# Kernel tuning notes

Hardware: AMD Instinct MI355X
Metric: run time of the kernel (lower is better)

## Reference

```python
import jax, jax.numpy as jnp
import numpy as np

EMB = 512
HEADS = 8
QKV = 512
WIN = 256  # 'range' init arg, >1 so W = range


def setup_inputs() -> dict:
    key = jax.random.key(0)
    ks = jax.random.split(key, 9)
    B, N = 2, 4096
    s_in = 1.0 / np.sqrt(EMB)
    s_qkv = 1.0 / np.sqrt(QKV)
    return {
        "x": jax.random.normal(ks[0], (B, N, EMB), jnp.float32),
        "Wq": jax.random.normal(ks[1], (EMB, QKV), jnp.float32) * s_in,
        "bq": jnp.zeros((QKV,), jnp.float32),
        "Wk": jax.random.normal(ks[2], (EMB, QKV), jnp.float32) * s_in,
        "bk": jnp.zeros((QKV,), jnp.float32),
        "Wv": jax.random.normal(ks[3], (EMB, QKV), jnp.float32) * s_in,
        "bv": jnp.zeros((QKV,), jnp.float32),
        "Wfc": jax.random.normal(ks[4], (QKV, EMB), jnp.float32) * s_qkv,
        "bfc": jnp.zeros((EMB,), jnp.float32),
    }


def reference(x, Wq, bq, Wk, bk, Wv, bv, Wfc, bfc):
    B, N, E = x.shape
    hd = QKV // HEADS  # head dim = 64
    # window mask: |i-j| <= W//2 -> 0 else -inf
    idx = jnp.arange(N)
    inwin = jnp.abs(idx[None, :] - idx[:, None]) <= (WIN // 2)
    M = jnp.where(inwin, 0.0, -jnp.inf).astype(x.dtype)  # [N,N]

    def split(h):  # [B,N,QKV] -> [B,H,N,hd]
        return h.reshape(B, N, HEADS, hd).transpose(0, 2, 1, 3)

    q = split(x @ Wq + bq)
    k = split(x @ Wk + bk)
    v = split(x @ Wv + bv)

    scale = 1.0 / np.sqrt(hd)
    attn = jnp.einsum("bhnd,bhmd->bhnm", q, k) * scale + M
    attn = jax.nn.softmax(attn, axis=-1)
    o = jnp.einsum("bhnm,bhmd->bhnd", attn, v)  # [B,H,N,hd]
    o = o.transpose(0, 2, 1, 3).reshape(B, N, QKV)
    return o @ Wfc + bfc
```

## Files before the change

kernel.cpp:

```cpp
#include <hip/hip_runtime.h>
#include <math.h>

typedef __bf16 bf16;
typedef __attribute__((ext_vector_type(8))) __bf16 bf16x8;
typedef __attribute__((ext_vector_type(4))) float f32x4;

#define N_SEQ 4096
#define NEGINF -1e30f

__device__ __forceinline__ void gl_lds16(const void* g, void* l) {
    __builtin_amdgcn_global_load_lds(
        (const __attribute__((address_space(1))) void*)g,
        (__attribute__((address_space(3))) void*)l, 16, 0, 0);
}

__device__ __forceinline__ bf16x8 frag64(const bf16* base, int row, int g) {
    return *(const bf16x8*)(base + (row << 6) + ((g ^ (row & 7)) << 3));
}

__global__ __launch_bounds__(256) void cast_x_k(const float* __restrict__ x,
                                                bf16* __restrict__ xb) {
    int idx = blockIdx.x * 256 + threadIdx.x;
    const float4* xv = (const float4*)x;
    float4 a = xv[idx * 2], b = xv[idx * 2 + 1];
    bf16x8 o;
    o[0] = (bf16)a.x; o[1] = (bf16)a.y; o[2] = (bf16)a.z; o[3] = (bf16)a.w;
    o[4] = (bf16)b.x; o[5] = (bf16)b.y; o[6] = (bf16)b.z; o[7] = (bf16)b.w;
    ((bf16x8*)xb)[idx] = o;
}

__global__ __launch_bounds__(256) void prep_w_k(
    const float* __restrict__ Wq, const float* __restrict__ bq,
    const float* __restrict__ Wk, const float* __restrict__ bk,
    const float* __restrict__ Wv, const float* __restrict__ bv,
    const float* __restrict__ Wfc, const float* __restrict__ bfc,
    bf16* __restrict__ Wcat, float* __restrict__ bcat) {
    const int t = threadIdx.x;
    const int k0 = blockIdx.x << 6, n0 = blockIdx.y << 6;
    const int sel = n0 >> 9, nloc = n0 & 511;
    const float* W = (sel == 0) ? Wq : (sel == 1) ? Wk : (sel == 2) ? Wv : Wfc;
    const float* bi = (sel == 0) ? bq : (sel == 1) ? bk : (sel == 2) ? bv : bfc;
    __shared__ bf16 tile[64][65];
#pragma unroll
    for (int i = 0; i < 16; i++) {
        int idx = (i << 8) + t;
        int r = idx >> 6, c = idx & 63;
        tile[r][c] = (bf16)W[(size_t)(k0 + r) * 512 + nloc + c];
    }
    __syncthreads();
#pragma unroll
    for (int i = 0; i < 16; i++) {
        int idx = (i << 8) + t;
        int r = idx >> 6, c = idx & 63;
        Wcat[(size_t)(n0 + r) * 512 + k0 + c] = tile[c][r];
    }
    if (blockIdx.x == 0 && t < 64) bcat[n0 + t] = bi[nloc + t];
}

template <int OUT, int BN>
__global__ __launch_bounds__(256) void gemm_bf16_k(
    const bf16* __restrict__ A, const bf16* __restrict__ Bt,
    const float* __restrict__ bias, void* __restrict__ Cout) {
    constexpr int NI = BN / 32;
    constexpr int BIT = BN / 32;
    __shared__ bf16 sA[2][128 * 64];
    __shared__ bf16 sB[2][BN * 64];
    const int t = threadIdx.x;
    const int lane = t & 63, wid = t >> 6;
    const int wr = wid >> 1, wc = wid & 1;
    const int m0 = blockIdx.x << 7;
    const int n0 = blockIdx.y * BN;

    f32x4 acc[4][NI] = {};

    const bf16* Ag = A + ((size_t)m0 << 9);
    const bf16* Bg = Bt + ((size_t)n0 << 9);

#define STAGE(buf, k0)                                                      \
    {                                                                       \
        _Pragma("unroll") for (int i = 0; i < 4; i++) {                     \
            int gid = (i << 8) + t;                                         \
            int row = gid >> 3, gs = ((gid & 7) ^ (row & 7)) << 3;          \
            gl_lds16(Ag + ((size_t)row << 9) + (k0) + gs, &sA[buf][gid << 3]); \
        }                                                                   \
        _Pragma("unroll") for (int i = 0; i < BIT; i++) {                   \
            int gid = (i << 8) + t;                                         \
            int row = gid >> 3, gs = ((gid & 7) ^ (row & 7)) << 3;          \
            gl_lds16(Bg + ((size_t)row << 9) + (k0) + gs, &sB[buf][gid << 3]); \
        }                                                                   \
    }

    STAGE(0, 0);
    __syncthreads();

    int buf = 0;
    for (int kt = 0; kt < 8; kt++) {
        if (kt < 7) STAGE(buf ^ 1, (kt + 1) << 6);
#pragma unroll
        for (int ks = 0; ks < 2; ks++) {
            int g = (ks << 2) + (lane >> 4);
            bf16x8 af[4], bfr[NI];
#pragma unroll
            for (int mi = 0; mi < 4; mi++)
                af[mi] = frag64(&sA[buf][0], (wr << 6) + (mi << 4) + (lane & 15), g);
#pragma unroll
            for (int ni = 0; ni < NI; ni++)
                bfr[ni] = frag64(&sB[buf][0], wc * (BN / 2) + (ni << 4) + (lane & 15), g);
#pragma unroll
            for (int mi = 0; mi < 4; mi++)
#pragma unroll
                for (int ni = 0; ni < NI; ni++)
                    acc[mi][ni] = __builtin_amdgcn_mfma_f32_16x16x32_bf16(
                        af[mi], bfr[ni], acc[mi][ni], 0, 0, 0);
        }
        __syncthreads();
        buf ^= 1;
    }
#undef STAGE

#pragma unroll
    for (int mi = 0; mi < 4; mi++) {
#pragma unroll
        for (int ni = 0; ni < NI; ni++) {
            int grow0 = m0 + (wr << 6) + (mi << 4) + ((lane >> 4) << 2);
            int gcol = n0 + wc * (BN / 2) + (ni << 4) + (lane & 15);
            float bb = bias[gcol];
#pragma unroll
            for (int r = 0; r < 4; r++) {
                int grow = grow0 + r;
                float v = acc[mi][ni][r] + bb;
                if (OUT == 0) {
                    int b = grow >> 12, n = grow & 4095;
                    int sel = gcol >> 9, rem = gcol & 511;
                    int h = rem >> 6, d = rem & 63;
                    size_t idx =
                        (((size_t)((sel << 4) + (b << 3) + h) * 4096 + n) << 6) + d;
                    ((bf16*)Cout)[idx] = (bf16)v;
                } else {
                    ((float*)Cout)[((size_t)grow << 9) + gcol] = v;
                }
            }
        }
    }
}

__global__ __launch_bounds__(256) void attn_bf16_k(
    const bf16* __restrict__ Q, const bf16* __restrict__ K,
    const bf16* __restrict__ V, bf16* __restrict__ O) {
    __shared__ bf16 QP[4096];
    __shared__ bf16 Ks[4096];
    __shared__ bf16 VT[4096];

    const int t = threadIdx.x;
    const int lane = t & 63, wid = t >> 6;
    const int bh = blockIdx.x >> 6;
    const int q0 = (blockIdx.x & 63) << 6;

    const bf16* Qp = Q + ((size_t)bh << 18);
    const bf16* Kp = K + ((size_t)bh << 18);
    const bf16* Vp = V + ((size_t)bh << 18);

#pragma unroll
    for (int i = 0; i < 2; i++) {
        int gid = (i << 8) + t;
        int row = gid >> 3, gs = ((gid & 7) ^ (row & 7)) << 3;
        gl_lds16(Qp + ((size_t)(q0 + row) << 6) + gs, &QP[gid << 3]);
    }
    __syncthreads();

    bf16x8 aq[2];
#pragma unroll
    for (int ks = 0; ks < 2; ks++)
        aq[ks] = frag64(QP, (wid << 4) + (lane & 15), (ks << 2) + (lane >> 4));

    float mrun[4], lrun[4];
    f32x4 acc_o[4] = {};
#pragma unroll
    for (int r = 0; r < 4; r++) { mrun[r] = NEGINF; lrun[r] = 0.f; }

    const int cstart = (q0 >= 128) ? q0 - 128 : 0;
    const int cend = (q0 + 192 <= N_SEQ) ? q0 + 192 : N_SEQ;
    bf16* Pw = &QP[wid << 10];

    for (int c0 = cstart; c0 < cend; c0 += 64) {
        __syncthreads();
#pragma unroll
        for (int i = 0; i < 2; i++) {
            int gid = (i << 8) + t;
            int row = gid >> 3, gs = ((gid & 7) ^ (row & 7)) << 3;
            gl_lds16(Kp + ((size_t)(c0 + row) << 6) + gs, &Ks[gid << 3]);
        }
        {
            int key = t >> 2;
            int gd0 = (t & 3) << 1;
            const uint4* vs = (const uint4*)(Vp + ((size_t)(c0 + key) << 6));
            union { uint4 u; bf16 h[8]; } u0, u1;
            u0.u = vs[gd0]; u1.u = vs[gd0 + 1];
#pragma unroll
            for (int e = 0; e < 8; e++) {
                int d0 = (gd0 << 3) + e;
                VT[(d0 << 6) + (((key >> 3) ^ (d0 & 7)) << 3) + (key & 7)] = u0.h[e];
                int d1 = d0 + 8;
                VT[(d1 << 6) + (((key >> 3) ^ (d1 & 7)) << 3) + (key & 7)] = u1.h[e];
            }
        }
        __syncthreads();

        f32x4 s[4] = {};
#pragma unroll
        for (int ks = 0; ks < 2; ks++) {
            int g = (ks << 2) + (lane >> 4);
#pragma unroll
            for (int ni = 0; ni < 4; ni++) {
                bf16x8 bk = frag64(Ks, (ni << 4) + (lane & 15), g);
                s[ni] = __builtin_amdgcn_mfma_f32_16x16x32_bf16(aq[ks], bk, s[ni], 0, 0, 0);
            }
        }

#pragma unroll
        for (int r = 0; r < 4; r++) {
            int rowl = ((lane >> 4) << 2) + r;
            int qi = q0 + (wid << 4) + rowl;
            float v[4];
#pragma unroll
            for (int ni = 0; ni < 4; ni++) {
                int kj = c0 + (ni << 4) + (lane & 15);
                int dd = qi - kj;
                v[ni] = (dd <= 128 && dd >= -128) ? s[ni][r] * 0.125f : NEGINF;
            }
            float mx = fmaxf(fmaxf(v[0], v[1]), fmaxf(v[2], v[3]));
#pragma unroll
            for (int off = 1; off < 16; off <<= 1)
                mx = fmaxf(mx, __shfl_xor(mx, off));
            float mn = fmaxf(mrun[r], mx);
            float alpha = __expf(mrun[r] - mn);
            float rs = 0.f;
#pragma unroll
            for (int ni = 0; ni < 4; ni++) {
                float p = __expf(v[ni] - mn);
                rs += p;
                int col = (ni << 4) + (lane & 15);
                Pw[(rowl << 6) + (((col >> 3) ^ (rowl & 7)) << 3) + (col & 7)] = (bf16)p;
            }
#pragma unroll
            for (int off = 1; off < 16; off <<= 1)
                rs += __shfl_xor(rs, off);
            mrun[r] = mn;
            lrun[r] = lrun[r] * alpha + rs;
#pragma unroll
            for (int nd = 0; nd < 4; nd++) acc_o[nd][r] *= alpha;
        }

#pragma unroll
        for (int ks = 0; ks < 2; ks++) {
            int g = (ks << 2) + (lane >> 4);
            bf16x8 pa = frag64(Pw, lane & 15, g);
#pragma unroll
            for (int nd = 0; nd < 4; nd++) {
                bf16x8 bv = frag64(VT, (nd << 4) + (lane & 15), g);
                acc_o[nd] = __builtin_amdgcn_mfma_f32_16x16x32_bf16(pa, bv, acc_o[nd], 0, 0, 0);
            }
        }
    }

    const int b = bh >> 3, h = bh & 7;
    float inv[4];
#pragma unroll
    for (int r = 0; r < 4; r++) inv[r] = 1.f / lrun[r];
#pragma unroll
    for (int nd = 0; nd < 4; nd++) {
#pragma unroll
        for (int r = 0; r < 4; r++) {
            int n = q0 + (wid << 4) + ((lane >> 4) << 2) + r;
            int d = (nd << 4) + (lane & 15);
            O[(((size_t)(b * 4096 + n)) << 9) + (h << 6) + d] =
                (bf16)(acc_o[nd][r] * inv[r]);
        }
    }
}

extern "C" void kernel_launch(void* const* d_in, const int* in_sizes, int n_in,
                              void* d_out, int out_size, void* d_ws, size_t ws_size,
                              hipStream_t stream) {
    (void)in_sizes; (void)n_in; (void)out_size; (void)ws_size;
    const float* x   = (const float*)d_in[0];
    const float* Wq  = (const float*)d_in[1];
    const float* bq  = (const float*)d_in[2];
    const float* Wk  = (const float*)d_in[3];
    const float* bk  = (const float*)d_in[4];
    const float* Wv  = (const float*)d_in[5];
    const float* bv  = (const float*)d_in[6];
    const float* Wfc = (const float*)d_in[7];
    const float* bfc = (const float*)d_in[8];

    bf16* xb    = (bf16*)d_ws;
    bf16* Wcat  = xb + (size_t)8192 * 512;
    float* bcat = (float*)(Wcat + (size_t)2048 * 512);
    bf16* QKVb  = (bf16*)(bcat + 2048);
    bf16* Ob    = QKVb + (size_t)3 * 16 * 4096 * 64;

    cast_x_k<<<(8192 * 512) / (256 * 8), 256, 0, stream>>>(x, xb);
    prep_w_k<<<dim3(8, 32), 256, 0, stream>>>(Wq, bq, Wk, bk, Wv, bv, Wfc, bfc,
                                              Wcat, bcat);

    gemm_bf16_k<0, 128><<<dim3(64, 12), 256, 0, stream>>>(xb, Wcat, bcat, QKVb);

    const bf16* Qb = QKVb;
    const bf16* Kb = QKVb + ((size_t)1 << 22);
    const bf16* Vb = QKVb + ((size_t)2 << 22);
    attn_bf16_k<<<1024, 256, 0, stream>>>(Qb, Kb, Vb, Ob);

    gemm_bf16_k<1, 64><<<dim3(64, 8), 256, 0, stream>>>(
        Ob, Wcat + ((size_t)1536 << 9), bcat + 1536, d_out);
}
```

Measured before the change: 148.1 us.

## Double-buffer K/V in attention, 128-query tiles, skip mask on diagonal chunks

```diff
diff --git a/kernel.cpp b/kernel.cpp
--- a/kernel.cpp
+++ b/kernel.cpp
@@ -147,134 +147,165 @@
 __global__ __launch_bounds__(256) void attn_bf16_k(
     const bf16* __restrict__ Q, const bf16* __restrict__ K,
     const bf16* __restrict__ V, bf16* __restrict__ O) {
-    __shared__ bf16 QP[4096];
-    __shared__ bf16 Ks[4096];
-    __shared__ bf16 VT[4096];
+    __shared__ bf16 QP[8192];
+    __shared__ bf16 Ks[2][4096];
+    __shared__ bf16 VT[2][4096];
 
     const int t = threadIdx.x;
     const int lane = t & 63, wid = t >> 6;
-    const int bh = blockIdx.x >> 6;
-    const int q0 = (blockIdx.x & 63) << 6;
+    const int bh = blockIdx.x >> 5;
+    const int q0 = (blockIdx.x & 31) << 7;
 
     const bf16* Qp = Q + ((size_t)bh << 18);
     const bf16* Kp = K + ((size_t)bh << 18);
     const bf16* Vp = V + ((size_t)bh << 18);
 
 #pragma unroll
-    for (int i = 0; i < 2; i++) {
+    for (int i = 0; i < 4; i++) {
         int gid = (i << 8) + t;
         int row = gid >> 3, gs = ((gid & 7) ^ (row & 7)) << 3;
         gl_lds16(Qp + ((size_t)(q0 + row) << 6) + gs, &QP[gid << 3]);
     }
     __syncthreads();
 
-    bf16x8 aq[2];
-#pragma unroll
-    for (int ks = 0; ks < 2; ks++)
-        aq[ks] = frag64(QP, (wid << 4) + (lane & 15), (ks << 2) + (lane >> 4));
-
-    float mrun[4], lrun[4];
-    f32x4 acc_o[4] = {};
-#pragma unroll
-    for (int r = 0; r < 4; r++) { mrun[r] = NEGINF; lrun[r] = 0.f; }
+    bf16x8 aq[2][2];
+#pragma unroll
+    for (int b = 0; b < 2; b++)
+#pragma unroll
+        for (int ks = 0; ks < 2; ks++)
+            aq[b][ks] = frag64(QP, (wid << 5) + (b << 4) + (lane & 15),
+                               (ks << 2) + (lane >> 4));
+
+    float mrun[2][4], lrun[2][4];
+    f32x4 acc_o[2][4] = {};
+#pragma unroll
+    for (int b = 0; b < 2; b++)
+#pragma unroll
+        for (int r = 0; r < 4; r++) { mrun[b][r] = NEGINF; lrun[b][r] = 0.f; }
 
     const int cstart = (q0 >= 128) ? q0 - 128 : 0;
-    const int cend = (q0 + 192 <= N_SEQ) ? q0 + 192 : N_SEQ;
-    bf16* Pw = &QP[wid << 10];
-
-    for (int c0 = cstart; c0 < cend; c0 += 64) {
+    const int cend = (q0 + 256 <= N_SEQ) ? q0 + 256 : N_SEQ;
+    const int nch = (cend - cstart) >> 6;
+
+#define STAGE_KV(c0, sb)                                                     \
+    {                                                                        \
+        _Pragma("unroll") for (int i = 0; i < 2; i++) {                      \
+            int gid = (i << 8) + t;                                          \
+            int row = gid >> 3, gs = ((gid & 7) ^ (row & 7)) << 3;           \
+            gl_lds16(Kp + ((size_t)((c0) + row) << 6) + gs,                  \
+                     &Ks[sb][gid << 3]);                                     \
+        }                                                                    \
+        int key = t >> 2;                                                    \
+        int gd0 = (t & 3) << 1;                                              \
+        const uint4* vs = (const uint4*)(Vp + ((size_t)((c0) + key) << 6));  \
+        union { uint4 u; bf16 h[8]; } u0, u1;                                \
+        u0.u = vs[gd0]; u1.u = vs[gd0 + 1];                                  \
+        _Pragma("unroll") for (int e = 0; e < 8; e++) {                      \
+            int d0 = (gd0 << 3) + e;                                         \
+            VT[sb][(d0 << 6) + (((key >> 3) ^ (d0 & 7)) << 3) + (key & 7)] = \
+                u0.h[e];                                                     \
+            int d1 = d0 + 8;                                                 \
+            VT[sb][(d1 << 6) + (((key >> 3) ^ (d1 & 7)) << 3) + (key & 7)] = \
+                u1.h[e];                                                     \
+        }                                                                    \
+    }
+
+    STAGE_KV(cstart, 0);
+
+    int buf = 0;
+    for (int tch = 0; tch < nch; tch++) {
+        const int c0 = cstart + (tch << 6);
         __syncthreads();
-#pragma unroll
-        for (int i = 0; i < 2; i++) {
-            int gid = (i << 8) + t;
-            int row = gid >> 3, gs = ((gid & 7) ^ (row & 7)) << 3;
-            gl_lds16(Kp + ((size_t)(c0 + row) << 6) + gs, &Ks[gid << 3]);
+        if (tch + 1 < nch) STAGE_KV(c0 + 64, buf ^ 1);
+
+        const int rel = c0 - q0;
+        const bool masked = (rel != 0) && (rel != 64);
+
+#pragma unroll
+        for (int b = 0; b < 2; b++) {
+            f32x4 s[4] = {};
+#pragma unroll
+            for (int ks = 0; ks < 2; ks++) {
+                int g = (ks << 2) + (lane >> 4);
+#pragma unroll
+                for (int ni = 0; ni < 4; ni++) {
+                    bf16x8 bk = frag64(&Ks[buf][0], (ni << 4) + (lane & 15), g);
+                    s[ni] = __builtin_amdgcn_mfma_f32_16x16x32_bf16(
+                        aq[b][ks], bk, s[ni], 0, 0, 0);
+                }
+            }
+
+            bf16* Pw = &QP[((wid << 1) + b) << 10];
+#pragma unroll
+            for (int r = 0; r < 4; r++) {
+                int rowl = ((lane >> 4) << 2) + r;
+                int qi = q0 + (wid << 5) + (b << 4) + rowl;
+                float v[4];
+                if (masked) {
+#pragma unroll
+                    for (int ni = 0; ni < 4; ni++) {
+                        int kj = c0 + (ni << 4) + (lane & 15);
+                        int dd = qi - kj;
+                        v[ni] = (dd <= 128 && dd >= -128) ? s[ni][r] * 0.125f
+                                                          : NEGINF;
+                    }
+                } else {
+#pragma unroll
+                    for (int ni = 0; ni < 4; ni++) v[ni] = s[ni][r] * 0.125f;
+                }
+                float mx = fmaxf(fmaxf(v[0], v[1]), fmaxf(v[2], v[3]));
+#pragma unroll
+                for (int off = 1; off < 16; off <<= 1)
+                    mx = fmaxf(mx, __shfl_xor(mx, off));
+                float mn = fmaxf(mrun[b][r], mx);
+                float alpha = __expf(mrun[b][r] - mn);
+                float rs = 0.f;
+#pragma unroll
+                for (int ni = 0; ni < 4; ni++) {
+                    float p = __expf(v[ni] - mn);
+                    rs += p;
+                    int col = (ni << 4) + (lane & 15);
+                    Pw[(rowl << 6) + (((col >> 3) ^ (rowl & 7)) << 3) +
+                       (col & 7)] = (bf16)p;
+                }
+#pragma unroll
+                for (int off = 1; off < 16; off <<= 1)
+                    rs += __shfl_xor(rs, off);
+                mrun[b][r] = mn;
+                lrun[b][r] = lrun[b][r] * alpha + rs;
+#pragma unroll
+                for (int nd = 0; nd < 4; nd++) acc_o[b][nd][r] *= alpha;
+            }
+
+#pragma unroll
+            for (int ks = 0; ks < 2; ks++) {
+                int g = (ks << 2) + (lane >> 4);
+                bf16x8 pa = frag64(Pw, lane & 15, g);
+#pragma unroll
+                for (int nd = 0; nd < 4; nd++) {
+                    bf16x8 bv = frag64(&VT[buf][0], (nd << 4) + (lane & 15), g);
+                    acc_o[b][nd] = __builtin_amdgcn_mfma_f32_16x16x32_bf16(
+                        pa, bv, acc_o[b][nd], 0, 0, 0);
+                }
+            }
         }
-        {
-            int key = t >> 2;
-            int gd0 = (t & 3) << 1;
-            const uint4* vs = (const uint4*)(Vp + ((size_t)(c0 + key) << 6));
-            union { uint4 u; bf16 h[8]; } u0, u1;
-            u0.u = vs[gd0]; u1.u = vs[gd0 + 1];
-#pragma unroll
-            for (int e = 0; e < 8; e++) {
-                int d0 = (gd0 << 3) + e;
-                VT[(d0 << 6) + (((key >> 3) ^ (d0 & 7)) << 3) + (key & 7)] = u0.h[e];
-                int d1 = d0 + 8;
-                VT[(d1 << 6) + (((key >> 3) ^ (d1 & 7)) << 3) + (key & 7)] = u1.h[e];
-            }
-        }
-        __syncthreads();
-
-        f32x4 s[4] = {};
-#pragma unroll
-        for (int ks = 0; ks < 2; ks++) {
-            int g = (ks << 2) + (lane >> 4);
-#pragma unroll
-            for (int ni = 0; ni < 4; ni++) {
-                bf16x8 bk = frag64(Ks, (ni << 4) + (lane & 15), g);
-                s[ni] = __builtin_amdgcn_mfma_f32_16x16x32_bf16(aq[ks], bk, s[ni], 0, 0, 0);
-            }
-        }
-
+        buf ^= 1;
+    }
+#undef STAGE_KV
+
+    const int bb = bh >> 3, h = bh & 7;
+#pragma unroll
+    for (int b = 0; b < 2; b++) {
 #pragma unroll
         for (int r = 0; r < 4; r++) {
-            int rowl = ((lane >> 4) << 2) + r;
-            int qi = q0 + (wid << 4) + rowl;
-            float v[4];
-#pragma unroll
-            for (int ni = 0; ni < 4; ni++) {
-                int kj = c0 + (ni << 4) + (lane & 15);
-                int dd = qi - kj;
-                v[ni] = (dd <= 128 && dd >= -128) ? s[ni][r] * 0.125f : NEGINF;
-            }
-            float mx = fmaxf(fmaxf(v[0], v[1]), fmaxf(v[2], v[3]));
-#pragma unroll
-            for (int off = 1; off < 16; off <<= 1)
-                mx = fmaxf(mx, __shfl_xor(mx, off));
-            float mn = fmaxf(mrun[r], mx);
-            float alpha = __expf(mrun[r] - mn);
-            float rs = 0.f;
-#pragma unroll
-            for (int ni = 0; ni < 4; ni++) {
-                float p = __expf(v[ni] - mn);
-                rs += p;
-                int col = (ni << 4) + (lane & 15);
-                Pw[(rowl << 6) + (((col >> 3) ^ (rowl & 7)) << 3) + (col & 7)] = (bf16)p;
-            }
-#pragma unroll
-            for (int off = 1; off < 16; off <<= 1)
-                rs += __shfl_xor(rs, off);
-            mrun[r] = mn;
-            lrun[r] = lrun[r] * alpha + rs;
-#pragma unroll
-            for (int nd = 0; nd < 4; nd++) acc_o[nd][r] *= alpha;
-        }
-
-#pragma unroll
-        for (int ks = 0; ks < 2; ks++) {
-            int g = (ks << 2) + (lane >> 4);
-            bf16x8 pa = frag64(Pw, lane & 15, g);
+            float inv = 1.f / lrun[b][r];
+            int n = q0 + (wid << 5) + (b << 4) + ((lane >> 4) << 2) + r;
 #pragma unroll
             for (int nd = 0; nd < 4; nd++) {
-                bf16x8 bv = frag64(VT, (nd << 4) + (lane & 15), g);
-                acc_o[nd] = __builtin_amdgcn_mfma_f32_16x16x32_bf16(pa, bv, acc_o[nd], 0, 0, 0);
-            }
-        }
-    }
-
-    const int b = bh >> 3, h = bh & 7;
-    float inv[4];
-#pragma unroll
-    for (int r = 0; r < 4; r++) inv[r] = 1.f / lrun[r];
-#pragma unroll
-    for (int nd = 0; nd < 4; nd++) {
-#pragma unroll
-        for (int r = 0; r < 4; r++) {
-            int n = q0 + (wid << 4) + ((lane >> 4) << 2) + r;
-            int d = (nd << 4) + (lane & 15);
-            O[(((size_t)(b * 4096 + n)) << 9) + (h << 6) + d] =
-                (bf16)(acc_o[nd][r] * inv[r]);
+                int d = (nd << 4) + (lane & 15);
+                O[(((size_t)(bb * 4096 + n)) << 9) + (h << 6) + d] =
+                    (bf16)(acc_o[b][nd][r] * inv);
+            }
         }
     }
 }
@@ -308,7 +339,7 @@
     const bf16* Qb = QKVb;
     const bf16* Kb = QKVb + ((size_t)1 << 22);
     const bf16* Vb = QKVb + ((size_t)2 << 22);
-    attn_bf16_k<<<1024, 256, 0, stream>>>(Qb, Kb, Vb, Ob);
+    attn_bf16_k<<<512, 256, 0, stream>>>(Qb, Kb, Vb, Ob);
 
     gemm_bf16_k<1, 64><<<dim3(64, 8), 256, 0, stream>>>(
         Ob, Wcat + ((size_t)1536 << 9), bcat + 1536, d_out);
```

New measurement: 155.0 us. +4.7%, slower.
